# Performance work log

Hardware: AMD Instinct MI355X
Metric: run time of the kernel (lower is better)

## Reference

```python
import jax, jax.numpy as jnp
import numpy as np

N = 50000      # nodes
E = 800000     # graph edges
NNZ = 800000   # hypergraph incidence entries
M = 10000      # hyperedges
IN, HID, OUT = 128, 64, 64


def setup_inputs() -> dict:
    key = jax.random.key(0)
    ks = jax.random.split(key, 12)
    x = jax.random.normal(ks[0], (N, IN), dtype=jnp.float32)
    edge_index = jax.random.randint(ks[1], (2, E), 0, N)
    node_idx = jax.random.randint(ks[2], (NNZ,), 0, N)
    he_idx = jax.random.randint(ks[3], (NNZ,), 0, M)
    hyperedge_index = jnp.stack([node_idx, he_idx])
    w = lambda k, fi, fo: jax.random.normal(k, (fi, fo), jnp.float32) / np.sqrt(fi)
    return {
        "x": x,
        "edge_index": edge_index,
        "hyperedge_index": hyperedge_index,
        "gcn1_w": w(ks[4], IN, HID), "gcn1_b": jnp.zeros((HID,), jnp.float32),
        "gcn2_w": w(ks[5], HID, OUT), "gcn2_b": jnp.zeros((OUT,), jnp.float32),
        "hyper1_w": w(ks[6], IN, HID), "hyper1_b": jnp.zeros((HID,), jnp.float32),
        "hyper2_w": w(ks[7], HID, OUT), "hyper2_b": jnp.zeros((OUT,), jnp.float32),
        "fusion_gate": jnp.zeros((1,), jnp.float32),
    }


def gcn_conv(x, edge_index, w, b):
    # PyG GCNConv: add self-loops, symmetric normalization, then aggregate.
    xw = x @ w
    loops = jnp.arange(N)
    row = jnp.concatenate([edge_index[0], loops])  # source j
    col = jnp.concatenate([edge_index[1], loops])  # target i
    deg = jax.ops.segment_sum(jnp.ones_like(col, dtype=xw.dtype), col, num_segments=N)
    dis = jnp.where(deg > 0, jax.lax.rsqrt(jnp.maximum(deg, 1e-12)), 0.0)
    norm = dis[row] * dis[col]
    out = jax.ops.segment_sum(norm[:, None] * xw[row], col, num_segments=N)
    return out + b


def hyper_conv(x, hyperedge_index, w, b):
    # PyG HypergraphConv (no attention, unit hyperedge weights):
    # out = D^{-1} H B^{-1} H^T (X W) + b
    xw = x @ w
    node_idx, he_idx = hyperedge_index[0], hyperedge_index[1]
    ones = jnp.ones((hyperedge_index.shape[1],), dtype=xw.dtype)
    D = jax.ops.segment_sum(ones, node_idx, num_segments=N)   # node degree
    B = jax.ops.segment_sum(ones, he_idx, num_segments=M)     # hyperedge degree
    Dinv = jnp.where(D > 0, 1.0 / jnp.maximum(D, 1e-12), 0.0)
    Binv = jnp.where(B > 0, 1.0 / jnp.maximum(B, 1e-12), 0.0)
    edge_feat = Binv[:, None] * jax.ops.segment_sum(xw[node_idx], he_idx, num_segments=M)
    out = Dinv[:, None] * jax.ops.segment_sum(edge_feat[he_idx], node_idx, num_segments=N)
    return out + b


def reference(x, edge_index, hyperedge_index,
              gcn1_w, gcn1_b, gcn2_w, gcn2_b,
              hyper1_w, hyper1_b, hyper2_w, hyper2_b,
              fusion_gate):
    # dropout is identity in eval mode (deterministic reference)
    x_s = gcn_conv(x, edge_index, gcn1_w, gcn1_b)
    x_s = jax.nn.elu(x_s)
    x_s = gcn_conv(x_s, edge_index, gcn2_w, gcn2_b)
    x_d = hyper_conv(x, hyperedge_index, hyper1_w, hyper1_b)
    x_d = jax.nn.elu(x_d)
    x_d = hyper_conv(x_d, hyperedge_index, hyper2_w, hyper2_b)
    alpha = jax.nn.sigmoid(fusion_gate)  # shape (1,), broadcasts
    z = alpha * x_s + (1.0 - alpha) * x_d
    return (z, x_s, x_d)
```

## Files before the change

kernel.cpp:

```cpp
#include <hip/hip_runtime.h>
#include <hip/hip_bf16.h>

#define N_NODES 50000
#define N_EDGES 800000
#define NNZ_H   800000
#define M_HE    10000
#define F_IN    128
#define F_HID   64

#define SH_E 7
#define NB_E ((N_NODES + 127) >> 7)
#define SH_H 5
#define NB_H ((M_HE + 31) >> 5)
#define SH_N 7
#define NB_N ((N_NODES + 127) >> 7)
#define TILE 4096
#define GB   ((N_EDGES + TILE - 1) / TILE)
#define NBMAX 400
#define KPBMAX 128
#define GG  782
#define GWN 12500

static __device__ __forceinline__ float bflo(unsigned v) { return __uint_as_float(v << 16); }
static __device__ __forceinline__ float bfhi(unsigned v) { return __uint_as_float(v & 0xFFFF0000u); }

__global__ void k_hist_all(const int* __restrict__ e_col, const int* __restrict__ h_idx,
                           const int* __restrict__ n_idx,
                           int* __restrict__ bcntE, int* __restrict__ bcntH, int* __restrict__ bcntN) {
    __shared__ int hE[NB_E], hH[NB_H], hN[NB_N];
    for (int i = threadIdx.x; i < NB_E; i += 256) hE[i] = 0;
    for (int i = threadIdx.x; i < NB_H; i += 256) hH[i] = 0;
    for (int i = threadIdx.x; i < NB_N; i += 256) hN[i] = 0;
    __syncthreads();
    const int2* ec2 = (const int2*)e_col;
    const int2* hi2 = (const int2*)h_idx;
    const int2* ni2 = (const int2*)n_idx;
    int stride = gridDim.x * 256;
    for (int i = blockIdx.x * 256 + threadIdx.x; i < N_EDGES / 2; i += stride) {
        int2 e = ec2[i];
        atomicAdd(&hE[e.x >> SH_E], 1);
        atomicAdd(&hE[e.y >> SH_E], 1);
        int2 hh = hi2[i];
        atomicAdd(&hH[hh.x >> SH_H], 1);
        atomicAdd(&hH[hh.y >> SH_H], 1);
        int2 nn = ni2[i];
        atomicAdd(&hN[nn.x >> SH_N], 1);
        atomicAdd(&hN[nn.y >> SH_N], 1);
    }
    __syncthreads();
    for (int i = threadIdx.x; i < NB_E; i += 256) if (hE[i]) atomicAdd(&bcntE[i], hE[i]);
    for (int i = threadIdx.x; i < NB_H; i += 256) if (hH[i]) atomicAdd(&bcntH[i], hH[i]);
    for (int i = threadIdx.x; i < NB_N; i += 256) if (hN[i]) atomicAdd(&bcntN[i], hN[i]);
}

__device__ void scan_to_lds(const int* __restrict__ in, int* __restrict__ soff, int nb,
                            int* __restrict__ tsum) {
    int t = threadIdx.x;
    int v0 = (2 * t < nb) ? in[2 * t] : 0;
    int v1 = (2 * t + 1 < nb) ? in[2 * t + 1] : 0;
    tsum[t] = v0 + v1;
    __syncthreads();
    for (int d = 1; d < 256; d <<= 1) {
        int u = (t >= d) ? tsum[t - d] : 0;
        __syncthreads();
        tsum[t] += u;
        __syncthreads();
    }
    int run = (t > 0) ? tsum[t - 1] : 0;
    if (2 * t < nb) soff[2 * t] = run;
    if (2 * t + 1 < nb) soff[2 * t + 1] = run + v0;
    __syncthreads();
}

__device__ void chunk_scatter(const int* __restrict__ keys, const int* __restrict__ vals,
                              int n, int sh, int nb,
                              const int* __restrict__ bcnt, int* __restrict__ bcur,
                              int* __restrict__ bk, int blk) {
    __shared__ int h[NBMAX], loc[NBMAX], base[NBMAX], hc[NBMAX], soff[NBMAX];
    __shared__ int tsum[256];
    __shared__ int buf[TILE];
    __shared__ unsigned short bkt[TILE];
    scan_to_lds(bcnt, soff, nb, tsum);
    int t0 = blk * TILE;
    int tend = min(t0 + TILE, n);
    int cnt = tend - t0;
    for (int b = threadIdx.x; b < nb; b += 256) { h[b] = 0; hc[b] = 0; }
    __syncthreads();
    for (int i = t0 + threadIdx.x; i < tend; i += 256)
        atomicAdd(&h[keys[i] >> sh], 1);
    __syncthreads();
    if (threadIdx.x == 0) {
        int run = 0;
        for (int b = 0; b < nb; ++b) { loc[b] = run; run += h[b]; }
    }
    __syncthreads();
    for (int b = threadIdx.x; b < nb; b += 256)
        base[b] = soff[b] + atomicAdd(&bcur[b], h[b]);
    __syncthreads();
    for (int i = t0 + threadIdx.x; i < tend; i += 256) {
        int k = keys[i];
        int b = k >> sh;
        int r = loc[b] + atomicAdd(&hc[b], 1);
        buf[r] = ((k - (b << sh)) << 16) | vals[i];
        bkt[r] = (unsigned short)b;
    }
    __syncthreads();
    for (int j = threadIdx.x; j < cnt; j += 256) {
        int b = bkt[j];
        bk[base[b] + (j - loc[b])] = buf[j];
    }
}
__global__ void k_chunk_all(const int* __restrict__ e_row, const int* __restrict__ e_col,
                            const int* __restrict__ n_idx, const int* __restrict__ h_idx,
                            const int* __restrict__ bcntE, int* __restrict__ bcurE, int* __restrict__ bkE,
                            const int* __restrict__ bcntH, int* __restrict__ bcurH, int* __restrict__ bkH,
                            const int* __restrict__ bcntN, int* __restrict__ bcurN, int* __restrict__ bkN) {
    int gb = blockIdx.x;
    if (gb < GB)            chunk_scatter(e_col, e_row, N_EDGES, SH_E, NB_E, bcntE, bcurE, bkE, gb);
    else if (gb < 2 * GB)   chunk_scatter(h_idx, n_idx, NNZ_H,  SH_H, NB_H, bcntH, bcurH, bkH, gb - GB);
    else                    chunk_scatter(n_idx, h_idx, NNZ_H,  SH_N, NB_N, bcntN, bcurN, bkN, gb - 2 * GB);
}

__global__ void k_fin_all(const int* __restrict__ bkE, const int* __restrict__ bcntE,
                          int* __restrict__ srtE, int* __restrict__ offE,
                          const int* __restrict__ bkH, const int* __restrict__ bcntH,
                          int* __restrict__ srtH, int* __restrict__ offH,
                          const int* __restrict__ bkN, const int* __restrict__ bcntN,
                          int* __restrict__ srtN, int* __restrict__ offN) {
    __shared__ int koff[KPBMAX];
    __shared__ int kcur[KPBMAX];
    __shared__ int tsum[256];
    __shared__ int soff[NBMAX];
    int b = blockIdx.x;
    const int* bk; const int* bcnt; int* srt; int* off;
    int nb, sh, nkeys, total;
    if (b < NB_E) {
        bk = bkE; bcnt = bcntE; srt = srtE; off = offE;
        nb = NB_E; sh = SH_E; nkeys = N_NODES; total = N_EDGES;
    } else if (b < NB_E + NB_H) {
        b -= NB_E;
        bk = bkH; bcnt = bcntH; srt = srtH; off = offH;
        nb = NB_H; sh = SH_H; nkeys = M_HE; total = NNZ_H;
    } else {
        b -= NB_E + NB_H;
        bk = bkN; bcnt = bcntN; srt = srtN; off = offN;
        nb = NB_N; sh = SH_N; nkeys = N_NODES; total = NNZ_H;
    }
    scan_to_lds(bcnt, soff, nb, tsum);
    int kpb = 1 << sh;
    int k0 = b << sh;
    int beg = soff[b];
    int end = (b + 1 < nb) ? soff[b + 1] : total;
    int t = threadIdx.x;
    if (t < kpb) { koff[t] = 0; kcur[t] = 0; }
    __syncthreads();
    for (int i = beg + t; i < end; i += 256)
        atomicAdd(&koff[((unsigned)bk[i]) >> 16], 1);
    __syncthreads();
    int v = (t < kpb) ? koff[t] : 0;
    tsum[t] = v;
    __syncthreads();
    for (int d = 1; d < 256; d <<= 1) {
        int u = (t >= d) ? tsum[t - d] : 0;
        __syncthreads();
        tsum[t] += u;
        __syncthreads();
    }
    if (t < kpb) koff[t] = tsum[t] - v;
    __syncthreads();
    if (t < kpb && (k0 + t) < nkeys) off[k0 + t] = beg + koff[t];
    if (b == nb - 1 && t == 0) off[nkeys] = total;
    for (int i = beg + t; i < end; i += 256) {
        int p = bk[i];
        int lk = ((unsigned)p) >> 16;
        int pos = beg + koff[lk] + atomicAdd(&kcur[lk], 1);
        srt[pos] = p & 0xFFFF;
    }
}

template<int K, bool SCALE>
__device__ __forceinline__ void gemm_body(const float* __restrict__ xin, const float* __restrict__ w,
                                          const int* __restrict__ offE, __hip_bfloat16* __restrict__ out,
                                          int blk, float* __restrict__ wl, float* __restrict__ xs) {
    int tid = threadIdx.x;
    int wv = tid >> 6, lane = tid & 63;
    int cg = lane & 15;
    int rg = lane >> 4;
    int rl = wv * 16 + rg * 4;
    int r0 = blk * 64;
    float acc[4][4] = {};
    for (int k0 = 0; k0 < K; k0 += 64) {
        {
            const float4* wsrc = (const float4*)(w + k0 * 64);
            float4* wdst = (float4*)wl;
            for (int j = tid; j < 1024; j += 256) wdst[j] = wsrc[j];
        }
        for (int p = tid; p < 1024; p += 256) {
            int r = p >> 4, c4 = p & 15;
            int row = min(r0 + r, N_NODES - 1);
            float4 vv = *(const float4*)(xin + (size_t)row * K + k0 + 4 * c4);
            *(float4*)&xs[r * 68 + 4 * c4] = vv;
        }
        __syncthreads();
#pragma unroll 4
        for (int kk = 0; kk < 64; ++kk) {
            float4 wf = *(const float4*)&wl[kk * 64 + cg * 4];
            float x0 = xs[(rl + 0) * 68 + kk];
            float x1 = xs[(rl + 1) * 68 + kk];
            float x2 = xs[(rl + 2) * 68 + kk];
            float x3 = xs[(rl + 3) * 68 + kk];
            acc[0][0] += x0 * wf.x; acc[0][1] += x0 * wf.y; acc[0][2] += x0 * wf.z; acc[0][3] += x0 * wf.w;
            acc[1][0] += x1 * wf.x; acc[1][1] += x1 * wf.y; acc[1][2] += x1 * wf.z; acc[1][3] += x1 * wf.w;
            acc[2][0] += x2 * wf.x; acc[2][1] += x2 * wf.y; acc[2][2] += x2 * wf.z; acc[2][3] += x2 * wf.w;
            acc[3][0] += x3 * wf.x; acc[3][1] += x3 * wf.y; acc[3][2] += x3 * wf.z; acc[3][3] += x3 * wf.w;
        }
        __syncthreads();
    }
#pragma unroll
    for (int i = 0; i < 4; ++i) {
        int row = r0 + rl + i;
        if (row < N_NODES) {
            float s = 1.0f;
            if (SCALE) {
                float deg = (float)(offE[row + 1] - offE[row]);
                s = rsqrtf(deg + 1.0f);
            }
            __hip_bfloat16 hv[4];
            hv[0] = __float2bfloat16(acc[i][0] * s);
            hv[1] = __float2bfloat16(acc[i][1] * s);
            hv[2] = __float2bfloat16(acc[i][2] * s);
            hv[3] = __float2bfloat16(acc[i][3] * s);
            *(ushort4*)&out[(size_t)row * 64 + cg * 4] = *(ushort4*)hv;
        }
    }
}

template<int K>
__global__ void k_gemm_dual(const float* __restrict__ in1, const float* __restrict__ w1,
                            const int* __restrict__ offE, __hip_bfloat16* __restrict__ out1,
                            const float* __restrict__ in2, const float* __restrict__ w2,
                            __hip_bfloat16* __restrict__ out2) {
    __shared__ float wl[64 * 64];
    __shared__ float xs[64 * 68];
    if (blockIdx.x < GG) gemm_body<K, true>(in1, w1, offE, out1, blockIdx.x, wl, xs);
    else                 gemm_body<K, false>(in2, w2, nullptr, out2, blockIdx.x - GG, wl, xs);
}

template<bool ELU>
__device__ __forceinline__ void gcn_gather_body(const int* __restrict__ off, const int* __restrict__ srcs,
                                                const __hip_bfloat16* __restrict__ xw,
                                                const float* __restrict__ b,
                                                float* __restrict__ out, int blk) {
    int tid = threadIdx.x;
    int wv = tid >> 6, lane = tid & 63;
    int h = lane >> 5, l = lane & 31;
    int wid = blk * 4 + wv;
    if (wid >= N_NODES) return;
    int beg = off[wid];
    int cnt = off[wid + 1] - beg;
    const unsigned* xwu = (const unsigned*)xw;
    float ax0 = 0, ay0 = 0, ax1 = 0, ay1 = 0, ax2 = 0, ay2 = 0, ax3 = 0, ay3 = 0;
    int k = h;
    for (; k + 14 < cnt; k += 16) {
        int s0 = srcs[beg + k],      s1 = srcs[beg + k + 2];
        int s2 = srcs[beg + k + 4],  s3 = srcs[beg + k + 6];
        int s4 = srcs[beg + k + 8],  s5 = srcs[beg + k + 10];
        int s6 = srcs[beg + k + 12], s7 = srcs[beg + k + 14];
        unsigned v0 = xwu[(size_t)s0 * 32 + l];
        unsigned v1 = xwu[(size_t)s1 * 32 + l];
        unsigned v2 = xwu[(size_t)s2 * 32 + l];
        unsigned v3 = xwu[(size_t)s3 * 32 + l];
        unsigned v4 = xwu[(size_t)s4 * 32 + l];
        unsigned v5 = xwu[(size_t)s5 * 32 + l];
        unsigned v6 = xwu[(size_t)s6 * 32 + l];
        unsigned v7 = xwu[(size_t)s7 * 32 + l];
        ax0 += bflo(v0); ay0 += bfhi(v0);
        ax1 += bflo(v1); ay1 += bfhi(v1);
        ax2 += bflo(v2); ay2 += bfhi(v2);
        ax3 += bflo(v3); ay3 += bfhi(v3);
        ax0 += bflo(v4); ay0 += bfhi(v4);
        ax1 += bflo(v5); ay1 += bfhi(v5);
        ax2 += bflo(v6); ay2 += bfhi(v6);
        ax3 += bflo(v7); ay3 += bfhi(v7);
    }
    for (; k + 6 < cnt; k += 8) {
        int s0 = srcs[beg + k],     s1 = srcs[beg + k + 2];
        int s2 = srcs[beg + k + 4], s3 = srcs[beg + k + 6];
        unsigned v0 = xwu[(size_t)s0 * 32 + l];
        unsigned v1 = xwu[(size_t)s1 * 32 + l];
        unsigned v2 = xwu[(size_t)s2 * 32 + l];
        unsigned v3 = xwu[(size_t)s3 * 32 + l];
        ax0 += bflo(v0); ay0 += bfhi(v0);
        ax1 += bflo(v1); ay1 += bfhi(v1);
        ax2 += bflo(v2); ay2 += bfhi(v2);
        ax3 += bflo(v3); ay3 += bfhi(v3);
    }
    for (; k < cnt; k += 2) {
        unsigned v = xwu[(size_t)srcs[beg + k] * 32 + l];
        ax0 += bflo(v); ay0 += bfhi(v);
    }
    float tx = (ax0 + ax1) + (ax2 + ax3);
    float ty = (ay0 + ay1) + (ay2 + ay3);
    tx += __shfl_xor(tx, 32);
    ty += __shfl_xor(ty, 32);
    unsigned sv = xwu[(size_t)wid * 32 + l];
    float di = rsqrtf((float)cnt + 1.0f);
    float vx = di * (tx + bflo(sv)) + b[2 * l];
    float vy = di * (ty + bfhi(sv)) + b[2 * l + 1];
    if (ELU) {
        vx = (vx > 0.0f) ? vx : expm1f(vx);
        vy = (vy > 0.0f) ? vy : expm1f(vy);
    }
    if (h == 0) *(float2*)(out + (size_t)wid * 64 + 2 * l) = make_float2(vx, vy);
}

__device__ __forceinline__ void he_gather_body(const int* __restrict__ off, const int* __restrict__ nodes,
                                               const __hip_bfloat16* __restrict__ xw,
                                               float* __restrict__ C, int he, float2 (*red)[32]) {
    int tid = threadIdx.x;
    int wv = tid >> 6, lane = tid & 63;
    int h = lane >> 5, l = lane & 31;
    int beg = off[he], end = off[he + 1];
    int cnt = end - beg;
    int per = (cnt + 3) >> 2;
    int b0 = beg + wv * per;
    int e0 = min(b0 + per, end);
    int c2 = e0 - b0;
    const unsigned* xwu = (const unsigned*)xw;
    float ax0 = 0, ay0 = 0, ax1 = 0, ay1 = 0, ax2 = 0, ay2 = 0, ax3 = 0, ay3 = 0;
    int k = h;
    for (; k + 14 < c2; k += 16) {
        int s0 = nodes[b0 + k],      s1 = nodes[b0 + k + 2];
        int s2 = nodes[b0 + k + 4],  s3 = nodes[b0 + k + 6];
        int s4 = nodes[b0 + k + 8],  s5 = nodes[b0 + k + 10];
        int s6 = nodes[b0 + k + 12], s7 = nodes[b0 + k + 14];
        unsigned v0 = xwu[(size_t)s0 * 32 + l];
        unsigned v1 = xwu[(size_t)s1 * 32 + l];
        unsigned v2 = xwu[(size_t)s2 * 32 + l];
        unsigned v3 = xwu[(size_t)s3 * 32 + l];
        unsigned v4 = xwu[(size_t)s4 * 32 + l];
        unsigned v5 = xwu[(size_t)s5 * 32 + l];
        unsigned v6 = xwu[(size_t)s6 * 32 + l];
        unsigned v7 = xwu[(size_t)s7 * 32 + l];
        ax0 += bflo(v0); ay0 += bfhi(v0);
        ax1 += bflo(v1); ay1 += bfhi(v1);
        ax2 += bflo(v2); ay2 += bfhi(v2);
        ax3 += bflo(v3); ay3 += bfhi(v3);
        ax0 += bflo(v4); ay0 += bfhi(v4);
        ax1 += bflo(v5); ay1 += bfhi(v5);
        ax2 += bflo(v6); ay2 += bfhi(v6);
        ax3 += bflo(v7); ay3 += bfhi(v7);
    }
    for (; k + 6 < c2; k += 8) {
        int s0 = nodes[b0 + k],     s1 = nodes[b0 + k + 2];
        int s2 = nodes[b0 + k + 4], s3 = nodes[b0 + k + 6];
        unsigned v0 = xwu[(size_t)s0 * 32 + l];
        unsigned v1 = xwu[(size_t)s1 * 32 + l];
        unsigned v2 = xwu[(size_t)s2 * 32 + l];
        unsigned v3 = xwu[(size_t)s3 * 32 + l];
        ax0 += bflo(v0); ay0 += bfhi(v0);
        ax1 += bflo(v1); ay1 += bfhi(v1);
        ax2 += bflo(v2); ay2 += bfhi(v2);
        ax3 += bflo(v3); ay3 += bfhi(v3);
    }
    for (; k < c2; k += 2) {
        unsigned v = xwu[(size_t)nodes[b0 + k] * 32 + l];
        ax0 += bflo(v); ay0 += bfhi(v);
    }
    float tx = (ax0 + ax1) + (ax2 + ax3);
    float ty = (ay0 + ay1) + (ay2 + ay3);
    tx += __shfl_xor(tx, 32);
    ty += __shfl_xor(ty, 32);
    if (h == 0) red[wv][l] = make_float2(tx, ty);
    __syncthreads();
    if (tid < 32) {
        float2 r0 = red[0][tid], r1 = red[1][tid], r2 = red[2][tid], r3 = red[3][tid];
        float binv = (cnt > 0) ? 1.0f / (float)cnt : 0.0f;
        float2 o = make_float2((r0.x + r1.x + r2.x + r3.x) * binv,
                               (r0.y + r1.y + r2.y + r3.y) * binv);
        *(float2*)(C + (size_t)he * 64 + 2 * tid) = o;
    }
}

template<bool ELU>
__global__ __launch_bounds__(256, 6)
void k_gather_dual(const int* __restrict__ offE, const int* __restrict__ srtE,
                   const __hip_bfloat16* __restrict__ A, const float* __restrict__ gb,
                   float* __restrict__ aggOut,
                   const int* __restrict__ offH, const int* __restrict__ srtH,
                   const __hip_bfloat16* __restrict__ B, float* __restrict__ C) {
    __shared__ float2 red[4][32];
    if (blockIdx.x < GWN) gcn_gather_body<ELU>(offE, srtE, A, gb, aggOut, blockIdx.x);
    else                  he_gather_body(offH, srtH, B, C, blockIdx.x - GWN, red);
}

template<bool ELU, bool FUSE>
__global__ __launch_bounds__(256, 8)
void k_node_gather(const int* __restrict__ off, const int* __restrict__ hes,
                   const float* __restrict__ C, const float* __restrict__ b,
                   float* __restrict__ out,
                   const float* __restrict__ xs, const float* __restrict__ gate,
                   float* __restrict__ z) {
    int tid = threadIdx.x;
    int wv = tid >> 6, lane = tid & 63;
    int h = lane >> 5, l = lane & 31;
    int wid = blockIdx.x * 4 + wv;
    if (wid >= N_NODES) return;
    int beg = off[wid];
    int cnt = off[wid + 1] - beg;
    float ax0 = 0, ay0 = 0, ax1 = 0, ay1 = 0, ax2 = 0, ay2 = 0, ax3 = 0, ay3 = 0;
    int k = h;
    for (; k + 6 < cnt; k += 8) {
        float2 c0 = *(const float2*)(C + (size_t)hes[beg + k] * 64 + 2 * l);
        float2 c1 = *(const float2*)(C + (size_t)hes[beg + k + 2] * 64 + 2 * l);
        float2 c2 = *(const float2*)(C + (size_t)hes[beg + k + 4] * 64 + 2 * l);
        float2 c3 = *(const float2*)(C + (size_t)hes[beg + k + 6] * 64 + 2 * l);
        ax0 += c0.x; ay0 += c0.y;
        ax1 += c1.x; ay1 += c1.y;
        ax2 += c2.x; ay2 += c2.y;
        ax3 += c3.x; ay3 += c3.y;
    }
    for (; k < cnt; k += 2) {
        float2 c = *(const float2*)(C + (size_t)hes[beg + k] * 64 + 2 * l);
        ax0 += c.x; ay0 += c.y;
    }
    float tx = (ax0 + ax1) + (ax2 + ax3);
    float ty = (ay0 + ay1) + (ay2 + ay3);
    tx += __shfl_xor(tx, 32);
    ty += __shfl_xor(ty, 32);
    float dinv = (cnt > 0) ? 1.0f / (float)cnt : 0.0f;
    float vx = dinv * tx + b[2 * l];
    float vy = dinv * ty + b[2 * l + 1];
    if (ELU) {
        vx = (vx > 0.0f) ? vx : expm1f(vx);
        vy = (vy > 0.0f) ? vy : expm1f(vy);
    }
    if (h == 0) {
        size_t idx = (size_t)wid * 64 + 2 * l;
        *(float2*)(out + idx) = make_float2(vx, vy);
        if (FUSE) {
            float a = 1.0f / (1.0f + expf(-gate[0]));
            float2 s = *(const float2*)(xs + idx);
            *(float2*)(z + idx) = make_float2(a * s.x + (1.0f - a) * vx,
                                              a * s.y + (1.0f - a) * vy);
        }
    }
}

extern "C" void kernel_launch(void* const* d_in, const int* in_sizes, int n_in,
                              void* d_out, int out_size, void* d_ws, size_t ws_size,
                              hipStream_t stream) {
    const float* x      = (const float*)d_in[0];
    const int*   ei     = (const int*)d_in[1];
    const int*   hei    = (const int*)d_in[2];
    const float* gcn1_w = (const float*)d_in[3];
    const float* gcn1_b = (const float*)d_in[4];
    const float* gcn2_w = (const float*)d_in[5];
    const float* gcn2_b = (const float*)d_in[6];
    const float* hyp1_w = (const float*)d_in[7];
    const float* hyp1_b = (const float*)d_in[8];
    const float* hyp2_w = (const float*)d_in[9];
    const float* hyp2_b = (const float*)d_in[10];
    const float* gate   = (const float*)d_in[11];
    float* out = (float*)d_out;

    const int* e_row = ei;
    const int* e_col = ei + N_EDGES;
    const int* n_idx = hei;
    const int* h_idx = hei + NNZ_H;

    const size_t NV = (size_t)N_NODES * 64;
    float* z_out  = out;
    float* xs_out = out + NV;
    float* xd_out = out + 2 * NV;

    char* base = (char*)d_ws;
    __hip_bfloat16* Abf = (__hip_bfloat16*)base;
    __hip_bfloat16* Bbf = (__hip_bfloat16*)(base + NV * 2);
    float* AGG1 = (float*)(base + NV * 4);
    float* AGG2 = (float*)(base + NV * 8);
    float* C    = (float*)(base + NV * 12);
    int* srtE = (int*)(C + (size_t)M_HE * 64);
    int* srtH = srtE + N_EDGES;
    int* srtN = srtH + NNZ_H;
    int* offE = srtN + NNZ_H;
    int* offH = offE + (N_NODES + 1);
    int* offN = offH + (M_HE + 1);
    int* bcntE = offN + (N_NODES + 1);
    int* bcntH = bcntE + NB_E;
    int* bcntN = bcntH + NB_H;
    int* bcurE = bcntN + NB_N;
    int* bcurH = bcurE + NB_E;
    int* bcurN = bcurH + NB_H;
    const size_t zero_ints = 2 * (size_t)(NB_E + NB_H + NB_N);
    int* bkE = (int*)Abf;
    int* bkH = (int*)Bbf;
    int* bkN = (int*)AGG1;

    const int BLK = 256;

    hipMemsetAsync(bcntE, 0, zero_ints * sizeof(int), stream);
    k_hist_all<<<256, BLK, 0, stream>>>(e_col, h_idx, n_idx, bcntE, bcntH, bcntN);
    k_chunk_all<<<3 * GB, BLK, 0, stream>>>(e_row, e_col, n_idx, h_idx,
                                            bcntE, bcurE, bkE,
                                            bcntH, bcurH, bkH,
                                            bcntN, bcurN, bkN);
    k_fin_all<<<NB_E + NB_H + NB_N, BLK, 0, stream>>>(bkE, bcntE, srtE, offE,
                                                      bkH, bcntH, srtH, offH,
                                                      bkN, bcntN, srtN, offN);

    k_gemm_dual<F_IN><<<2 * GG, BLK, 0, stream>>>(x, gcn1_w, offE, Abf, x, hyp1_w, Bbf);
    k_gather_dual<true><<<GWN + M_HE, BLK, 0, stream>>>(offE, srtE, Abf, gcn1_b, AGG1,
                                                        offH, srtH, Bbf, C);
    k_node_gather<true, false><<<GWN, BLK, 0, stream>>>(offN, srtN, C, hyp1_b, AGG2,
                                                        nullptr, nullptr, nullptr);
    k_gemm_dual<F_HID><<<2 * GG, BLK, 0, stream>>>(AGG1, gcn2_w, offE, Abf, AGG2, hyp2_w, Bbf);
    k_gather_dual<false><<<GWN + M_HE, BLK, 0, stream>>>(offE, srtE, Abf, gcn2_b, xs_out,
                                                         offH, srtH, Bbf, C);
    k_node_gather<false, true><<<GWN, BLK, 0, stream>>>(offN, srtN, C, hyp2_b, xd_out,
                                                        xs_out, gate, z_out);

    (void)in_sizes; (void)n_in; (void)out_size; (void)ws_size;
}
```

Before: 259.9 us.

## Use nontemporal loads/stores for streaming data and transpose GEMM smem tile

Marks streaming index reads and output writes with nontemporal hints so they avoid polluting cache needed for the randomly gathered feature rows. The dense-transform kernel now stores the input tile transposed in shared memory so each thread reads four row values with one float4 load. The trade-off is that global input loads become scalar nontemporal loads instead of float4, and the transposed shared stores may cause bank conflicts.

```diff
diff --git a/kernel.cpp b/kernel.cpp
--- a/kernel.cpp
+++ b/kernel.cpp
@@ -21,8 +21,15 @@
 #define GG  782
 #define GWN 12500
 
+typedef float nf2 __attribute__((ext_vector_type(2)));
+
 static __device__ __forceinline__ float bflo(unsigned v) { return __uint_as_float(v << 16); }
 static __device__ __forceinline__ float bfhi(unsigned v) { return __uint_as_float(v & 0xFFFF0000u); }
+#define NTL(p) __builtin_nontemporal_load(p)
+static __device__ __forceinline__ void nts2(float* p, float x, float y) {
+    nf2 v; v.x = x; v.y = y;
+    __builtin_nontemporal_store(v, (nf2*)p);
+}
 
 __global__ void k_hist_all(const int* __restrict__ e_col, const int* __restrict__ h_idx,
                            const int* __restrict__ n_idx,
@@ -198,21 +205,25 @@
         for (int p = tid; p < 1024; p += 256) {
             int r = p >> 4, c4 = p & 15;
             int row = min(r0 + r, N_NODES - 1);
-            float4 vv = *(const float4*)(xin + (size_t)row * K + k0 + 4 * c4);
-            *(float4*)&xs[r * 68 + 4 * c4] = vv;
+            const float* src = xin + (size_t)row * K + k0 + 4 * c4;
+            float v0 = NTL(src + 0);
+            float v1 = NTL(src + 1);
+            float v2 = NTL(src + 2);
+            float v3 = NTL(src + 3);
+            xs[(4 * c4 + 0) * 68 + r] = v0;
+            xs[(4 * c4 + 1) * 68 + r] = v1;
+            xs[(4 * c4 + 2) * 68 + r] = v2;
+            xs[(4 * c4 + 3) * 68 + r] = v3;
         }
         __syncthreads();
 #pragma unroll 4
         for (int kk = 0; kk < 64; ++kk) {
             float4 wf = *(const float4*)&wl[kk * 64 + cg * 4];
-            float x0 = xs[(rl + 0) * 68 + kk];
-            float x1 = xs[(rl + 1) * 68 + kk];
-            float x2 = xs[(rl + 2) * 68 + kk];
-            float x3 = xs[(rl + 3) * 68 + kk];
-            acc[0][0] += x0 * wf.x; acc[0][1] += x0 * wf.y; acc[0][2] += x0 * wf.z; acc[0][3] += x0 * wf.w;
-            acc[1][0] += x1 * wf.x; acc[1][1] += x1 * wf.y; acc[1][2] += x1 * wf.z; acc[1][3] += x1 * wf.w;
-            acc[2][0] += x2 * wf.x; acc[2][1] += x2 * wf.y; acc[2][2] += x2 * wf.z; acc[2][3] += x2 * wf.w;
-            acc[3][0] += x3 * wf.x; acc[3][1] += x3 * wf.y; acc[3][2] += x3 * wf.z; acc[3][3] += x3 * wf.w;
+            float4 xf = *(const float4*)&xs[kk * 68 + rl];
+            acc[0][0] += xf.x * wf.x; acc[0][1] += xf.x * wf.y; acc[0][2] += xf.x * wf.z; acc[0][3] += xf.x * wf.w;
+            acc[1][0] += xf.y * wf.x; acc[1][1] += xf.y * wf.y; acc[1][2] += xf.y * wf.z; acc[1][3] += xf.y * wf.w;
+            acc[2][0] += xf.z * wf.x; acc[2][1] += xf.z * wf.y; acc[2][2] += xf.z * wf.z; acc[2][3] += xf.z * wf.w;
+            acc[3][0] += xf.w * wf.x; acc[3][1] += xf.w * wf.y; acc[3][2] += xf.w * wf.z; acc[3][3] += xf.w * wf.w;
         }
         __syncthreads();
     }
@@ -262,10 +273,10 @@
     float ax0 = 0, ay0 = 0, ax1 = 0, ay1 = 0, ax2 = 0, ay2 = 0, ax3 = 0, ay3 = 0;
     int k = h;
     for (; k + 14 < cnt; k += 16) {
-        int s0 = srcs[beg + k],      s1 = srcs[beg + k + 2];
-        int s2 = srcs[beg + k + 4],  s3 = srcs[beg + k + 6];
-        int s4 = srcs[beg + k + 8],  s5 = srcs[beg + k + 10];
-        int s6 = srcs[beg + k + 12], s7 = srcs[beg + k + 14];
+        int s0 = NTL(&srcs[beg + k]),      s1 = NTL(&srcs[beg + k + 2]);
+        int s2 = NTL(&srcs[beg + k + 4]),  s3 = NTL(&srcs[beg + k + 6]);
+        int s4 = NTL(&srcs[beg + k + 8]),  s5 = NTL(&srcs[beg + k + 10]);
+        int s6 = NTL(&srcs[beg + k + 12]), s7 = NTL(&srcs[beg + k + 14]);
         unsigned v0 = xwu[(size_t)s0 * 32 + l];
         unsigned v1 = xwu[(size_t)s1 * 32 + l];
         unsigned v2 = xwu[(size_t)s2 * 32 + l];
@@ -284,8 +295,8 @@
         ax3 += bflo(v7); ay3 += bfhi(v7);
     }
     for (; k + 6 < cnt; k += 8) {
-        int s0 = srcs[beg + k],     s1 = srcs[beg + k + 2];
-        int s2 = srcs[beg + k + 4], s3 = srcs[beg + k + 6];
+        int s0 = NTL(&srcs[beg + k]),     s1 = NTL(&srcs[beg + k + 2]);
+        int s2 = NTL(&srcs[beg + k + 4]), s3 = NTL(&srcs[beg + k + 6]);
         unsigned v0 = xwu[(size_t)s0 * 32 + l];
         unsigned v1 = xwu[(size_t)s1 * 32 + l];
         unsigned v2 = xwu[(size_t)s2 * 32 + l];
@@ -296,7 +307,7 @@
         ax3 += bflo(v3); ay3 += bfhi(v3);
     }
     for (; k < cnt; k += 2) {
-        unsigned v = xwu[(size_t)srcs[beg + k] * 32 + l];
+        unsigned v = xwu[(size_t)NTL(&srcs[beg + k]) * 32 + l];
         ax0 += bflo(v); ay0 += bfhi(v);
     }
     float tx = (ax0 + ax1) + (ax2 + ax3);
@@ -311,7 +322,7 @@
         vx = (vx > 0.0f) ? vx : expm1f(vx);
         vy = (vy > 0.0f) ? vy : expm1f(vy);
     }
-    if (h == 0) *(float2*)(out + (size_t)wid * 64 + 2 * l) = make_float2(vx, vy);
+    if (h == 0) nts2(out + (size_t)wid * 64 + 2 * l, vx, vy);
 }
 
 __device__ __forceinline__ void he_gather_body(const int* __restrict__ off, const int* __restrict__ nodes,
@@ -330,10 +341,10 @@
     float ax0 = 0, ay0 = 0, ax1 = 0, ay1 = 0, ax2 = 0, ay2 = 0, ax3 = 0, ay3 = 0;
     int k = h;
     for (; k + 14 < c2; k += 16) {
-        int s0 = nodes[b0 + k],      s1 = nodes[b0 + k + 2];
-        int s2 = nodes[b0 + k + 4],  s3 = nodes[b0 + k + 6];
-        int s4 = nodes[b0 + k + 8],  s5 = nodes[b0 + k + 10];
-        int s6 = nodes[b0 + k + 12], s7 = nodes[b0 + k + 14];
+        int s0 = NTL(&nodes[b0 + k]),      s1 = NTL(&nodes[b0 + k + 2]);
+        int s2 = NTL(&nodes[b0 + k + 4]),  s3 = NTL(&nodes[b0 + k + 6]);
+        int s4 = NTL(&nodes[b0 + k + 8]),  s5 = NTL(&nodes[b0 + k + 10]);
+        int s6 = NTL(&nodes[b0 + k + 12]), s7 = NTL(&nodes[b0 + k + 14]);
         unsigned v0 = xwu[(size_t)s0 * 32 + l];
         unsigned v1 = xwu[(size_t)s1 * 32 + l];
         unsigned v2 = xwu[(size_t)s2 * 32 + l];
@@ -352,8 +363,8 @@
         ax3 += bflo(v7); ay3 += bfhi(v7);
     }
     for (; k + 6 < c2; k += 8) {
-        int s0 = nodes[b0 + k],     s1 = nodes[b0 + k + 2];
-        int s2 = nodes[b0 + k + 4], s3 = nodes[b0 + k + 6];
+        int s0 = NTL(&nodes[b0 + k]),     s1 = NTL(&nodes[b0 + k + 2]);
+        int s2 = NTL(&nodes[b0 + k + 4]), s3 = NTL(&nodes[b0 + k + 6]);
         unsigned v0 = xwu[(size_t)s0 * 32 + l];
         unsigned v1 = xwu[(size_t)s1 * 32 + l];
         unsigned v2 = xwu[(size_t)s2 * 32 + l];
@@ -364,7 +375,7 @@
         ax3 += bflo(v3); ay3 += bfhi(v3);
     }
     for (; k < c2; k += 2) {
-        unsigned v = xwu[(size_t)nodes[b0 + k] * 32 + l];
+        unsigned v = xwu[(size_t)NTL(&nodes[b0 + k]) * 32 + l];
         ax0 += bflo(v); ay0 += bfhi(v);
     }
     float tx = (ax0 + ax1) + (ax2 + ax3);
@@ -376,9 +387,9 @@
     if (tid < 32) {
         float2 r0 = red[0][tid], r1 = red[1][tid], r2 = red[2][tid], r3 = red[3][tid];
         float binv = (cnt > 0) ? 1.0f / (float)cnt : 0.0f;
-        float2 o = make_float2((r0.x + r1.x + r2.x + r3.x) * binv,
-                               (r0.y + r1.y + r2.y + r3.y) * binv);
-        *(float2*)(C + (size_t)he * 64 + 2 * tid) = o;
+        *(float2*)(C + (size_t)he * 64 + 2 * tid) =
+            make_float2((r0.x + r1.x + r2.x + r3.x) * binv,
+                        (r0.y + r1.y + r2.y + r3.y) * binv);
     }
 }
 
@@ -411,17 +422,19 @@
     float ax0 = 0, ay0 = 0, ax1 = 0, ay1 = 0, ax2 = 0, ay2 = 0, ax3 = 0, ay3 = 0;
     int k = h;
     for (; k + 6 < cnt; k += 8) {
-        float2 c0 = *(const float2*)(C + (size_t)hes[beg + k] * 64 + 2 * l);
-        float2 c1 = *(const float2*)(C + (size_t)hes[beg + k + 2] * 64 + 2 * l);
-        float2 c2 = *(const float2*)(C + (size_t)hes[beg + k + 4] * 64 + 2 * l);
-        float2 c3 = *(const float2*)(C + (size_t)hes[beg + k + 6] * 64 + 2 * l);
+        int s0 = NTL(&hes[beg + k]),     s1 = NTL(&hes[beg + k + 2]);
+        int s2 = NTL(&hes[beg + k + 4]), s3 = NTL(&hes[beg + k + 6]);
+        float2 c0 = *(const float2*)(C + (size_t)s0 * 64 + 2 * l);
+        float2 c1 = *(const float2*)(C + (size_t)s1 * 64 + 2 * l);
+        float2 c2 = *(const float2*)(C + (size_t)s2 * 64 + 2 * l);
+        float2 c3 = *(const float2*)(C + (size_t)s3 * 64 + 2 * l);
         ax0 += c0.x; ay0 += c0.y;
         ax1 += c1.x; ay1 += c1.y;
         ax2 += c2.x; ay2 += c2.y;
         ax3 += c3.x; ay3 += c3.y;
     }
     for (; k < cnt; k += 2) {
-        float2 c = *(const float2*)(C + (size_t)hes[beg + k] * 64 + 2 * l);
+        float2 c = *(const float2*)(C + (size_t)NTL(&hes[beg + k]) * 64 + 2 * l);
         ax0 += c.x; ay0 += c.y;
     }
     float tx = (ax0 + ax1) + (ax2 + ax3);
@@ -437,12 +450,11 @@
     }
     if (h == 0) {
         size_t idx = (size_t)wid * 64 + 2 * l;
-        *(float2*)(out + idx) = make_float2(vx, vy);
+        nts2(out + idx, vx, vy);
         if (FUSE) {
             float a = 1.0f / (1.0f + expf(-gate[0]));
             float2 s = *(const float2*)(xs + idx);
-            *(float2*)(z + idx) = make_float2(a * s.x + (1.0f - a) * vx,
-                                              a * s.y + (1.0f - a) * vy);
+            nts2(z + idx, a * s.x + (1.0f - a) * vx, a * s.y + (1.0f - a) * vy);
         }
     }
 }
```

Result: slower. 300.8 us (+15.7%).
